# Performance work log

Hardware: AMD Instinct MI355X
Metric: run time of the kernel (lower is better)

Reference implementation:

```python
import jax, jax.numpy as jnp
import numpy as np

HEAD = 4
HW_DIM = 256  # in_dim // 2


def _gconv1x1(x, w, b):
    # groups=2 pointwise conv: x [B,C,H,W], w [O, C//2], b [O]
    B, C, H, W = x.shape
    O = w.shape[0]
    xg = x.reshape(B, 2, C // 2, H, W)
    wg = w.reshape(2, O // 2, C // 2)
    y = jnp.einsum('bgchw,goc->bgohw', xg, wg).reshape(B, O, H, W)
    return y + b[None, :, None, None]


def _bn_train(x, w, b, eps=1e-5):
    # BatchNorm2d in training mode (batch statistics over N,H,W)
    mean = x.mean(axis=(0, 2, 3), keepdims=True)
    var = ((x - mean) ** 2).mean(axis=(0, 2, 3), keepdims=True)
    return (x - mean) / jnp.sqrt(var + eps) * w[None, :, None, None] + b[None, :, None, None]


def _forward(x, wq, bq, wk, bk, wv, bv, bnh_w, bnh_b, bnw_w, bnw_b, gamma):
    B, C, H, W = x.shape
    org_x = x
    # first half of channels is detached in the original forward
    xd = jnp.concatenate([jax.lax.stop_gradient(x[:, :HW_DIM]), x[:, HW_DIM:]], axis=1)

    dqk_h = 512 // HEAD  # 128 per-head qk dim == `long`
    dv_h = 256 // HEAD   # 64 per-head value dim
    q = _gconv1x1(xd, wq, bq).reshape(B, HEAD, dqk_h, H, W)
    k = _gconv1x1(xd, wk, bk).reshape(B, HEAD, dqk_h, H, W)
    v = _gconv1x1(xd, wv, bv).reshape(B, HEAD, dv_h, H, W)
    scale = dqk_h ** (-0.5)

    # --- attention along H (per width column) ---
    eH = jnp.einsum('bnciw,bncjw->bnwij', q, k) * scale  # [B,HEAD,W,H,H]
    aH = jax.nn.softmax(eH, axis=-1)
    out_H = jnp.einsum('bnwij,bncjw->bnciw', aH, v).reshape(B, HEAD * dv_h, H, W)

    # --- attention along W (per height row) ---
    eW = jnp.einsum('bnchi,bnchj->bnhij', q, k) * scale  # [B,HEAD,H,W,W]
    aW = jax.nn.softmax(eW, axis=-1)
    out_W = jnp.einsum('bnhij,bnchj->bnchi', aW, v).reshape(B, HEAD * dv_h, H, W)

    p0 = _bn_train(out_H, bnh_w, bnh_b)[:, :HW_DIM // 2]
    p1 = _bn_train(out_W, bnw_w, bnw_b)[:, :HW_DIM // 2]

    out_temp = jnp.concatenate([out_H, out_W], axis=1)  # pre-BN outputs
    out = gamma * jax.nn.relu(out_temp) + org_x
    return out, p0, p1


def setup_inputs() -> dict:
    key = jax.random.key(0)
    ks = jax.random.split(key, 4)
    B, C, H, W = 4, 512, 128, 128
    s = 0.02
    return {
        'x': jax.random.normal(ks[0], (B, C, H, W), jnp.float32),
        'wq': jax.random.normal(ks[1], (512, 256), jnp.float32) * s,
        'bq': jnp.zeros((512,), jnp.float32),
        'wk': jax.random.normal(ks[2], (512, 256), jnp.float32) * s,
        'bk': jnp.zeros((512,), jnp.float32),
        'wv': jax.random.normal(ks[3], (256, 256), jnp.float32) * s,
        'bv': jnp.zeros((256,), jnp.float32),
        'bnh_w': jnp.ones((256,), jnp.float32),
        'bnh_b': jnp.zeros((256,), jnp.float32),
        'bnw_w': jnp.ones((256,), jnp.float32),
        'bnw_b': jnp.zeros((256,), jnp.float32),
        'gamma': jnp.full((1,), 0.1, jnp.float32),
    }


def reference(x, wq, bq, wk, bk, wv, bv, bnh_w, bnh_b, bnw_w, bnw_b, gamma):
    return _forward(x, wq, bq, wk, bk, wv, bv, bnh_w, bnh_b, bnw_w, bnw_b, gamma)
```

## Files before the change

kernel.cpp:

```cpp
#include <hip/hip_runtime.h>
#include <cstdint>
#include <cstddef>

constexpr int Bn = 4, Cin = 512, Hn = 128, Wn = 128, HWn = Hn * Wn;
constexpr float SCALE_LOG2E = 0.12751743f;
constexpr float INV_CNT = 1.52587890625e-05f;

typedef unsigned short u16;
typedef unsigned int u32;
using f32x4  = __attribute__((ext_vector_type(4))) float;
using bf16x8 = __attribute__((ext_vector_type(8))) short;

#define MFMA(a, b, c) __builtin_amdgcn_mfma_f32_16x16x32_bf16((a), (b), (c), 0, 0, 0)

__device__ __forceinline__ u16 bfu(float f) {
  u32 u = __float_as_uint(f);
  u += 0x7fffu + ((u >> 16) & 1u);
  return (u16)(u >> 16);
}

constexpr size_t SZ_XT = (size_t)Bn * HWn * 512 * 2;
constexpr size_t SZ_QK = (size_t)Bn * 4 * HWn * 128 * 2;
constexpr size_t SZ_V  = (size_t)Bn * 4 * HWn * 64 * 2;
constexpr size_t SZ_O  = (size_t)Bn * 256 * HWn * 4;
constexpr size_t OFF_XT = 0;
constexpr size_t OFF_Q  = OFF_XT + SZ_XT;
constexpr size_t OFF_K  = OFF_Q + SZ_QK;
constexpr size_t OFF_V  = OFF_K + SZ_QK;
constexpr size_t OFF_OH = OFF_V + SZ_V;
constexpr size_t OFF_OW = OFF_OH + SZ_O;
constexpr size_t OFF_ST = OFF_OW + SZ_O;
constexpr size_t OFF_WB = OFF_ST + 4096;
constexpr size_t OFF_BB = OFF_WB + (size_t)1280 * 256 * 2;

__global__ __launch_bounds__(256) void k_transpose_cast(
    const float* __restrict__ x,
    const float* __restrict__ wq, const float* __restrict__ wk, const float* __restrict__ wv,
    const float* __restrict__ bq, const float* __restrict__ bk, const float* __restrict__ bv,
    u16* __restrict__ xT, u16* __restrict__ Wb, float* __restrict__ Bb) {
  __shared__ float tile[32][33];
  const int t = threadIdx.x;
  if (blockIdx.z == 4) {
    if (blockIdx.y == 0 && blockIdx.x < 320) {
      int idx = (blockIdx.x * 256 + t) * 4;
      int row = idx >> 8, col = idx & 255;
      const float* src = (row < 512)  ? (wq + (size_t)row * 256 + col)
                       : (row < 1024) ? (wk + (size_t)(row - 512) * 256 + col)
                                      : (wv + (size_t)(row - 1024) * 256 + col);
      float4 v = *(const float4*)src;
      u32 lo = (u32)bfu(v.x) | ((u32)bfu(v.y) << 16);
      u32 hi = (u32)bfu(v.z) | ((u32)bfu(v.w) << 16);
      *(uint2*)&Wb[idx] = make_uint2(lo, hi);
    } else if (blockIdx.y == 1 && blockIdx.x == 0) {
      for (int i = t; i < 1280; i += 256)
        Bb[i] = (i < 512) ? bq[i] : (i < 1024) ? bk[i - 512] : bv[i - 1024];
    }
    return;
  }
  const int b = blockIdx.z, c0 = blockIdx.y * 32, p0 = blockIdx.x * 32;
  const int pi = t & 31, ci = t >> 5;
  const float* xp = x + ((size_t)b * Cin + c0) * HWn + p0;
  for (int cc = ci; cc < 32; cc += 8) tile[cc][pi] = xp[(size_t)cc * HWn + pi];
  __syncthreads();
  u16* o = xT + ((size_t)b * HWn + p0) * Cin + c0;
  for (int pp = ci; pp < 32; pp += 8) o[(size_t)pp * Cin + pi] = bfu(tile[pi][pp]);
}

__global__ __launch_bounds__(256, 3) void k_proj(
    const u16* __restrict__ xT, const u16* __restrict__ Wb, const float* __restrict__ Bb,
    u16* __restrict__ Q, u16* __restrict__ K, u16* __restrict__ V,
    float* __restrict__ stats) {
  __shared__ u16 xs[128 * 128];

  const int t = threadIdx.x;
  const int ot = blockIdx.x;
  const int pos0 = blockIdx.y * 128;
  const int b = blockIdx.z;

  if (ot == 0 && blockIdx.y == 0 && b == 0) { stats[t] = 0.f; stats[256 + t] = 0.f; }

  const int g = (ot < 8) ? ((ot & 3) >> 1) : (ot - 8);
  const u16* xrow = xT + ((size_t)b * HWn + pos0) * 512 + g * 256;

  const int lane = t & 63, wid = t >> 6, ln = lane & 15, qd = lane >> 4;
  const u16* wr0 = Wb + ((size_t)ot * 128 + wid * 32 + ln) * 256;

  f32x4 acc[2][8];
#pragma unroll
  for (int mi = 0; mi < 2; ++mi)
#pragma unroll
    for (int nt = 0; nt < 8; ++nt) acc[mi][nt] = f32x4{0.f, 0.f, 0.f, 0.f};

  for (int kc = 0; kc < 2; ++kc) {
    __syncthreads();
#pragma unroll
    for (int p = 0; p < 8; ++p) {
      int id = p * 256 + t;
      int pos = id >> 4, kb = id & 15;
      uint4 v = *(const uint4*)(xrow + (size_t)pos * 512 + kc * 128 + kb * 8);
      *(uint4*)&xs[pos * 128 + (kb ^ (pos & 15)) * 8] = v;
    }
    __syncthreads();
    bf16x8 a[2][4];
#pragma unroll
    for (int kk = 0; kk < 4; ++kk) {
      int kbi = kk * 4 + qd;
      a[0][kk] = *(const bf16x8*)(wr0 + kc * 128 + kbi * 8);
      a[1][kk] = *(const bf16x8*)(wr0 + 16 * 256 + kc * 128 + kbi * 8);
    }
#pragma unroll
    for (int kk = 0; kk < 4; ++kk) {
      int kbi = kk * 4 + qd;
#pragma unroll
      for (int nt = 0; nt < 8; ++nt) {
        bf16x8 bf_ = *(const bf16x8*)(xs + (nt * 16 + ln) * 128 + (kbi ^ ln) * 8);
        acc[0][nt] = MFMA(a[0][kk], bf_, acc[0][nt]);
        acc[1][nt] = MFMA(a[1][kk], bf_, acc[1][nt]);
      }
    }
  }
  __syncthreads();
#pragma unroll
  for (int mi = 0; mi < 2; ++mi) {
    int oc = wid * 32 + mi * 16 + qd * 4;
    const float* bp = Bb + ot * 128 + oc;
    float b0 = bp[0], b1 = bp[1], b2 = bp[2], b3 = bp[3];
    int ocb = oc >> 2;
#pragma unroll
    for (int nt = 0; nt < 8; ++nt) {
      int pos = nt * 16 + ln;
      u32 lo = (u32)bfu(acc[mi][nt][0] + b0) | ((u32)bfu(acc[mi][nt][1] + b1) << 16);
      u32 hi = (u32)bfu(acc[mi][nt][2] + b2) | ((u32)bfu(acc[mi][nt][3] + b3) << 16);
      *(uint2*)&xs[pos * 128 + ((ocb ^ (pos & 31)) << 2)] = make_uint2(lo, hi);
    }
  }
  __syncthreads();
  if (ot < 8) {
    u16* dst = (ot < 4) ? Q + (size_t)(b * 4 + ot) * HWn * 128
                        : K + (size_t)(b * 4 + (ot - 4)) * HWn * 128;
#pragma unroll
    for (int p = 0; p < 8; ++p) {
      int id = p * 256 + t;
      int pos = id >> 4, grp = id & 15;
      int s0 = (grp * 2) ^ (pos & 31), s1 = (grp * 2 + 1) ^ (pos & 31);
      uint2 g0 = *(const uint2*)&xs[pos * 128 + (s0 << 2)];
      uint2 g1 = *(const uint2*)&xs[pos * 128 + (s1 << 2)];
      *(uint4*)(dst + (size_t)(pos0 + pos) * 128 + grp * 8) = make_uint4(g0.x, g0.y, g1.x, g1.y);
    }
  } else {
    u16* vb = V + (size_t)(b * 4 + (ot - 8) * 2) * HWn * 64;
#pragma unroll
    for (int p = 0; p < 8; ++p) {
      int id = p * 256 + t;
      int pos = id >> 4, grp = id & 15;
      int off = grp * 8;
      int s0 = (grp * 2) ^ (pos & 31), s1 = (grp * 2 + 1) ^ (pos & 31);
      uint2 g0 = *(const uint2*)&xs[pos * 128 + (s0 << 2)];
      uint2 g1 = *(const uint2*)&xs[pos * 128 + (s1 << 2)];
      u16* d = vb + (size_t)((off >> 6) * HWn + pos0 + pos) * 64 + (off & 63);
      *(uint4*)d = make_uint4(g0.x, g0.y, g1.x, g1.y);
    }
  }
}

__global__ __launch_bounds__(256) void k_attn(
    const u16* __restrict__ Qg, const u16* __restrict__ Kg, const u16* __restrict__ Vg,
    float* __restrict__ outH, float* __restrict__ outW, float* __restrict__ stats) {
  __shared__ u16 sm[64 * 128 + 128 * 128];
  u16* VT = sm;
  u16* KP = sm + 64 * 128;
  float* Os = (float*)KP;
  float* scr = (float*)VT;

  const int t = threadIdx.x;
  const int s = blockIdx.x;
  const int b = blockIdx.y >> 2, n = blockIdx.y & 3;
  const int dir = blockIdx.z;
  const int pos_base = (dir == 0) ? s : s * 128;
  const int step = (dir == 0) ? 128 : 1;

  const u16* qb = Qg + (size_t)(b * 4 + n) * HWn * 128;
  const u16* kb = Kg + (size_t)(b * 4 + n) * HWn * 128;
  const u16* vb = Vg + (size_t)(b * 4 + n) * HWn * 64;

#pragma unroll
  for (int p = 0; p < 8; ++p) {
    int id = p * 256 + t;
    int row = id >> 4, kk = id & 15;
    uint4 v = *(const uint4*)(kb + (size_t)(pos_base + row * step) * 128 + kk * 8);
    *(uint4*)&KP[row * 128 + (kk ^ (row & 15)) * 8] = v;
  }
#pragma unroll
  for (int p = 0; p < 4; ++p) {
    int id = p * 256 + t;
    int j = id >> 3, cb = id & 7;
    uint4 v = *(const uint4*)(vb + (size_t)(pos_base + j * step) * 64 + cb * 8);
    const u16* pv = (const u16*)&v;
    int jb = j >> 3, jr = j & 7;
#pragma unroll
    for (int e = 0; e < 8; ++e) {
      int c = cb * 8 + e;
      VT[c * 128 + (((jb ^ (c & 15)) << 3) | jr)] = pv[e];
    }
  }
  __syncthreads();

  const int lane = t & 63, wid = t >> 6, ln = lane & 15, qd = lane >> 4;
  f32x4 accS[2][8];
#pragma unroll
  for (int mi = 0; mi < 2; ++mi)
#pragma unroll
    for (int nt = 0; nt < 8; ++nt) accS[mi][nt] = f32x4{0.f, 0.f, 0.f, 0.f};

#pragma unroll
  for (int kk = 0; kk < 4; ++kk) {
    int kbi = kk * 4 + qd;
    bf16x8 a0 = *(const bf16x8*)(qb + (size_t)(pos_base + (wid * 32 + ln) * step) * 128 + kbi * 8);
    bf16x8 a1 = *(const bf16x8*)(qb + (size_t)(pos_base + (wid * 32 + 16 + ln) * step) * 128 + kbi * 8);
#pragma unroll
    for (int nt = 0; nt < 8; ++nt) {
      int row = nt * 16 + ln;
      bf16x8 bf_ = *(const bf16x8*)(KP + row * 128 + (kbi ^ ln) * 8);
      accS[0][nt] = MFMA(a0, bf_, accS[0][nt]);
      accS[1][nt] = MFMA(a1, bf_, accS[1][nt]);
    }
  }
  float rinv[2][4];
#pragma unroll
  for (int mi = 0; mi < 2; ++mi)
#pragma unroll
    for (int r = 0; r < 4; ++r) {
      float mx = accS[mi][0][r];
#pragma unroll
      for (int nt = 1; nt < 8; ++nt) mx = fmaxf(mx, accS[mi][nt][r]);
      mx = fmaxf(mx, __shfl_xor(mx, 1));
      mx = fmaxf(mx, __shfl_xor(mx, 2));
      mx = fmaxf(mx, __shfl_xor(mx, 4));
      mx = fmaxf(mx, __shfl_xor(mx, 8));
      float sum = 0.f;
#pragma unroll
      for (int nt = 0; nt < 8; ++nt) {
        float e = exp2f((accS[mi][nt][r] - mx) * SCALE_LOG2E);
        accS[mi][nt][r] = e; sum += e;
      }
      sum += __shfl_xor(sum, 1);
      sum += __shfl_xor(sum, 2);
      sum += __shfl_xor(sum, 4);
      sum += __shfl_xor(sum, 8);
      rinv[mi][r] = __builtin_amdgcn_rcpf(sum);
    }
  __syncthreads();
#pragma unroll
  for (int mi = 0; mi < 2; ++mi) {
    int mbase = (wid * 2 + mi) * 16 + qd * 4;
#pragma unroll
    for (int nt = 0; nt < 8; ++nt) {
      int nb = nt * 2 + (ln >> 3), nr = ln & 7;
#pragma unroll
      for (int r = 0; r < 4; ++r) {
        int m = mbase + r;
        KP[m * 128 + (((nb ^ (m & 15)) << 3) | nr)] = bfu(accS[mi][nt][r]);
      }
    }
  }
  f32x4 accO[2][4];
#pragma unroll
  for (int mi = 0; mi < 2; ++mi)
#pragma unroll
    for (int nt = 0; nt < 4; ++nt) accO[mi][nt] = f32x4{0.f, 0.f, 0.f, 0.f};
#pragma unroll
  for (int jj = 0; jj < 4; ++jj) {
    int jb2 = jj * 4 + qd;
    bf16x8 a0 = *(const bf16x8*)(KP + (wid * 32 + ln) * 128 + (jb2 ^ ln) * 8);
    bf16x8 a1 = *(const bf16x8*)(KP + (wid * 32 + 16 + ln) * 128 + (jb2 ^ ln) * 8);
#pragma unroll
    for (int nt = 0; nt < 4; ++nt) {
      int c = nt * 16 + ln;
      bf16x8 bf_ = *(const bf16x8*)(VT + c * 128 + (jb2 ^ (c & 15)) * 8);
      accO[0][nt] = MFMA(a0, bf_, accO[0][nt]);
      accO[1][nt] = MFMA(a1, bf_, accO[1][nt]);
    }
  }
  __syncthreads();
  float s1[4] = {0.f, 0.f, 0.f, 0.f}, s2[4] = {0.f, 0.f, 0.f, 0.f};
#pragma unroll
  for (int mi = 0; mi < 2; ++mi) {
    int ib = ((wid * 2 + mi) * 16 + qd * 4) >> 2;
#pragma unroll
    for (int nt = 0; nt < 4; ++nt) {
      int c = nt * 16 + ln;
      f32x4 v;
#pragma unroll
      for (int r = 0; r < 4; ++r) v[r] = accO[mi][nt][r] * rinv[mi][r];
      if (n < 2) {
#pragma unroll
        for (int r = 0; r < 4; ++r) { s1[nt] += v[r]; s2[nt] += v[r] * v[r]; }
      }
      *(f32x4*)(Os + c * 128 + ((ib ^ (c & 31)) << 2)) = v;
    }
  }
  if (n < 2) {
#pragma unroll
    for (int nt = 0; nt < 4; ++nt) {
      float a = s1[nt]; a += __shfl_xor(a, 16); a += __shfl_xor(a, 32);
      float q2 = s2[nt]; q2 += __shfl_xor(q2, 16); q2 += __shfl_xor(q2, 32);
      if (qd == 0) {
        scr[(wid * 2 + 0) * 64 + nt * 16 + ln] = a;
        scr[(wid * 2 + 1) * 64 + nt * 16 + ln] = q2;
      }
    }
  }
  __syncthreads();
  if (n < 2 && t < 128) {
    int part = t >> 6, c2 = t & 63;
    float v = scr[(0 * 2 + part) * 64 + c2] + scr[(1 * 2 + part) * 64 + c2] +
              scr[(2 * 2 + part) * 64 + c2] + scr[(3 * 2 + part) * 64 + c2];
    atomicAdd(&stats[dir * 256 + part * 128 + n * 64 + c2], v);
  }
  float* obase; size_t cstride;
  if (dir == 0) { obase = outH + ((size_t)(b * 4 + n) * 128 + s) * 8192; cstride = 128; }
  else          { obase = outW + (size_t)(b * 256 + n * 64) * HWn + (size_t)s * 128; cstride = HWn; }
#pragma unroll
  for (int p = 0; p < 8; ++p) {
    int id = p * 256 + t;
    int c = id >> 5, i4 = id & 31;
    f32x4 v = *(const f32x4*)(Os + c * 128 + ((i4 ^ (c & 31)) << 2));
    *(f32x4*)(obase + (size_t)c * cstride + i4 * 4) = v;
  }
}

__global__ __launch_bounds__(256) void k_final(
    const float* __restrict__ x, const float* __restrict__ outH,
    const float* __restrict__ outW, const float* __restrict__ stats,
    const float* __restrict__ bnh_w, const float* __restrict__ bnh_b,
    const float* __restrict__ bnw_w, const float* __restrict__ bnw_b,
    const float* __restrict__ gamma,
    float* __restrict__ out, float* __restrict__ p0, float* __restrict__ p1) {
  __shared__ float lds[32 * 129];
  const int t = threadIdx.x;
  const int w0 = blockIdx.x * 32;
  const int ch = blockIdx.y;
  const int b = blockIdx.z;
  const float gm = gamma[0];
  const float* xp = x + (size_t)(b * 512 + ch) * HWn;
  float* op = out + (size_t)(b * 512 + ch) * HWn;
  if (ch < 256) {
    const int n = ch >> 6, c = ch & 63;
    const float* hb = outH + (size_t)(b * 4 + n) * 128 * 8192 + c * 128;
    for (int ps = 0; ps < 16; ++ps) {
      int wl = ps * 2 + (t >> 7);
      lds[wl * 129 + (t & 127)] = hb[(size_t)(w0 + wl) * 8192 + (t & 127)];
    }
    __syncthreads();
    const bool dop = ch < 128;
    float mean = 0.f, istd = 0.f, bw = 0.f, bb = 0.f;
    if (dop) {
      mean = stats[ch] * INV_CNT;
      float ex2 = stats[128 + ch] * INV_CNT;
      istd = rsqrtf(fmaxf(ex2 - mean * mean, 0.f) + 1e-5f);
      bw = bnh_w[ch]; bb = bnh_b[ch];
    }
    float* pp = p0 + (size_t)(b * 128 + ch) * HWn;
    const int w = t & 31, h0 = t >> 5;
    for (int hh = 0; hh < 16; ++hh) {
      int h = hh * 8 + h0;
      float v = lds[w * 129 + h];
      int gi = h * 128 + w0 + w;
      op[gi] = gm * fmaxf(v, 0.f) + xp[gi];
      if (dop) pp[gi] = (v - mean) * istd * bw + bb;
    }
  } else {
    const int cw = ch - 256;
    const float* wbp = outW + (size_t)(b * 256 + cw) * HWn;
    const bool dop = cw < 128;
    float mean = 0.f, istd = 0.f, bw = 0.f, bb = 0.f;
    if (dop) {
      mean = stats[256 + cw] * INV_CNT;
      float ex2 = stats[384 + cw] * INV_CNT;
      istd = rsqrtf(fmaxf(ex2 - mean * mean, 0.f) + 1e-5f);
      bw = bnw_w[cw]; bb = bnw_b[cw];
    }
    float* pp = p1 + (size_t)(b * 128 + cw) * HWn;
    for (int it = 0; it < 16; ++it) {
      int fl = it * 256 + t;
      int h = fl >> 5, w = fl & 31;
      int gi = h * 128 + w0 + w;
      float v = wbp[gi];
      op[gi] = gm * fmaxf(v, 0.f) + xp[gi];
      if (dop) pp[gi] = (v - mean) * istd * bw + bb;
    }
  }
}

extern "C" void kernel_launch(void* const* d_in, const int* in_sizes, int n_in,
                              void* d_out, int out_size, void* d_ws, size_t ws_size,
                              hipStream_t stream) {
  (void)in_sizes; (void)n_in; (void)out_size; (void)ws_size;
  const float* x    = (const float*)d_in[0];
  const float* wq   = (const float*)d_in[1];
  const float* bq   = (const float*)d_in[2];
  const float* wk   = (const float*)d_in[3];
  const float* bk   = (const float*)d_in[4];
  const float* wv   = (const float*)d_in[5];
  const float* bv   = (const float*)d_in[6];
  const float* bnhw = (const float*)d_in[7];
  const float* bnhb = (const float*)d_in[8];
  const float* bnww = (const float*)d_in[9];
  const float* bnwb = (const float*)d_in[10];
  const float* gamma = (const float*)d_in[11];

  char* ws = (char*)d_ws;
  u16* xT = (u16*)(ws + OFF_XT);
  u16* Q  = (u16*)(ws + OFF_Q);
  u16* K  = (u16*)(ws + OFF_K);
  u16* V  = (u16*)(ws + OFF_V);
  float* oH = (float*)(ws + OFF_OH);
  float* oW = (float*)(ws + OFF_OW);
  float* st = (float*)(ws + OFF_ST);
  u16* Wb = (u16*)(ws + OFF_WB);
  float* Bb = (float*)(ws + OFF_BB);

  float* out = (float*)d_out;
  float* p0 = out + (size_t)Bn * 512 * HWn;
  float* p1 = p0 + (size_t)Bn * 128 * HWn;

  k_transpose_cast<<<dim3(512, 16, 5), 256, 0, stream>>>(x, wq, wk, wv, bq, bk, bv, xT, Wb, Bb);
  k_proj<<<dim3(10, 128, 4), 256, 0, stream>>>(xT, Wb, Bb, Q, K, V, st);
  k_attn<<<dim3(128, 16, 2), 256, 0, stream>>>(Q, K, V, oH, oW, st);
  k_final<<<dim3(4, 512, 4), 256, 0, stream>>>(x, oH, oW, st, bnhw, bnhb, bnww, bnwb, gamma,
                                               out, p0, p1);
}
```

Before: 577.5 us.

## Fuse W-direction residual epilogue into attention, use direct global-to-LDS loads, remap proj blocks

The W-direction attention now writes the gamma*relu+x output directly and stores raw pre-BN values only for the first 128 channels. The final kernel no longer processes the upper 128 W channels and handles the BN-only path with vectorized loads. K and projection input tiles are copied to LDS with global_load_lds, with the XOR swizzle applied on the global address side. Projection blocks are remapped so neighbouring blocks spread across XCDs. Together these cut HBM traffic for the outW round trip and some register staging, at the cost of more complex index mapping.

```diff
diff --git a/kernel.cpp b/kernel.cpp
--- a/kernel.cpp
+++ b/kernel.cpp
@@ -17,6 +17,12 @@
   u32 u = __float_as_uint(f);
   u += 0x7fffu + ((u >> 16) & 1u);
   return (u16)(u >> 16);
+}
+
+__device__ __forceinline__ void gload_lds16(const void* g, void* l) {
+  __builtin_amdgcn_global_load_lds(
+      (const __attribute__((address_space(1))) u32*)g,
+      (__attribute__((address_space(3))) u32*)l, 16, 0, 0);
 }
 
 constexpr size_t SZ_XT = (size_t)Bn * HWn * 512 * 2;
@@ -73,11 +79,14 @@
   __shared__ u16 xs[128 * 128];
 
   const int t = threadIdx.x;
-  const int ot = blockIdx.x;
-  const int pos0 = blockIdx.y * 128;
-  const int b = blockIdx.z;
-
-  if (ot == 0 && blockIdx.y == 0 && b == 0) { stats[t] = 0.f; stats[256 + t] = 0.f; }
+  const int flat = blockIdx.x + 10 * (blockIdx.y + (blockIdx.z << 7));
+  const int work = ((flat & 7) * 640) + (flat >> 3);
+  const int ot = work % 10;
+  const int rest = work / 10;
+  const int b = rest >> 7;
+  const int pos0 = (rest & 127) << 7;
+
+  if (work == 0) { stats[t] = 0.f; stats[256 + t] = 0.f; }
 
   const int g = (ot < 8) ? ((ot & 3) >> 1) : (ot - 8);
   const u16* xrow = xT + ((size_t)b * HWn + pos0) * 512 + g * 256;
@@ -97,10 +106,9 @@
     for (int p = 0; p < 8; ++p) {
       int id = p * 256 + t;
       int pos = id >> 4, kb = id & 15;
-      uint4 v = *(const uint4*)(xrow + (size_t)pos * 512 + kc * 128 + kb * 8);
-      *(uint4*)&xs[pos * 128 + (kb ^ (pos & 15)) * 8] = v;
-    }
-    __syncthreads();
+      gload_lds16(xrow + (size_t)pos * 512 + kc * 128 + ((kb ^ (pos & 15)) << 3),
+                  xs + id * 8);
+    }
     bf16x8 a[2][4];
 #pragma unroll
     for (int kk = 0; kk < 4; ++kk) {
@@ -108,6 +116,7 @@
       a[0][kk] = *(const bf16x8*)(wr0 + kc * 128 + kbi * 8);
       a[1][kk] = *(const bf16x8*)(wr0 + 16 * 256 + kc * 128 + kbi * 8);
     }
+    __syncthreads();
 #pragma unroll
     for (int kk = 0; kk < 4; ++kk) {
       int kbi = kk * 4 + qd;
@@ -165,7 +174,9 @@
 
 __global__ __launch_bounds__(256) void k_attn(
     const u16* __restrict__ Qg, const u16* __restrict__ Kg, const u16* __restrict__ Vg,
-    float* __restrict__ outH, float* __restrict__ outW, float* __restrict__ stats) {
+    const float* __restrict__ x, const float* __restrict__ gamma,
+    float* __restrict__ outH, float* __restrict__ oWraw, float* __restrict__ out,
+    float* __restrict__ stats) {
   __shared__ u16 sm[64 * 128 + 128 * 128];
   u16* VT = sm;
   u16* KP = sm + 64 * 128;
@@ -187,8 +198,8 @@
   for (int p = 0; p < 8; ++p) {
     int id = p * 256 + t;
     int row = id >> 4, kk = id & 15;
-    uint4 v = *(const uint4*)(kb + (size_t)(pos_base + row * step) * 128 + kk * 8);
-    *(uint4*)&KP[row * 128 + (kk ^ (row & 15)) * 8] = v;
+    gload_lds16(kb + (size_t)(pos_base + row * step) * 128 + ((kk ^ (row & 15)) << 3),
+                KP + id * 8);
   }
 #pragma unroll
   for (int p = 0; p < 4; ++p) {
@@ -317,21 +328,38 @@
               scr[(2 * 2 + part) * 64 + c2] + scr[(3 * 2 + part) * 64 + c2];
     atomicAdd(&stats[dir * 256 + part * 128 + n * 64 + c2], v);
   }
-  float* obase; size_t cstride;
-  if (dir == 0) { obase = outH + ((size_t)(b * 4 + n) * 128 + s) * 8192; cstride = 128; }
-  else          { obase = outW + (size_t)(b * 256 + n * 64) * HWn + (size_t)s * 128; cstride = HWn; }
-#pragma unroll
-  for (int p = 0; p < 8; ++p) {
-    int id = p * 256 + t;
-    int c = id >> 5, i4 = id & 31;
-    f32x4 v = *(const f32x4*)(Os + c * 128 + ((i4 ^ (c & 31)) << 2));
-    *(f32x4*)(obase + (size_t)c * cstride + i4 * 4) = v;
+  if (dir == 0) {
+    float* obase = outH + ((size_t)(b * 4 + n) * 128 + s) * 8192;
+#pragma unroll
+    for (int p = 0; p < 8; ++p) {
+      int id = p * 256 + t;
+      int c = id >> 5, i4 = id & 31;
+      f32x4 v = *(const f32x4*)(Os + c * 128 + ((i4 ^ (c & 31)) << 2));
+      *(f32x4*)(obase + (size_t)c * 128 + i4 * 4) = v;
+    }
+  } else {
+    const float gm = gamma[0];
+    const float* xb = x + ((size_t)b * 512 + 256 + n * 64) * HWn + (size_t)s * 128;
+    float* ob = out + ((size_t)b * 512 + 256 + n * 64) * HWn + (size_t)s * 128;
+    float* rb = oWraw + ((size_t)b * 128 + n * 64) * HWn + (size_t)s * 128;
+#pragma unroll
+    for (int p = 0; p < 8; ++p) {
+      int id = p * 256 + t;
+      int c = id >> 5, i4 = id & 31;
+      f32x4 v = *(const f32x4*)(Os + c * 128 + ((i4 ^ (c & 31)) << 2));
+      f32x4 xv = *(const f32x4*)(xb + (size_t)c * HWn + i4 * 4);
+      f32x4 o;
+#pragma unroll
+      for (int r = 0; r < 4; ++r) o[r] = gm * fmaxf(v[r], 0.f) + xv[r];
+      *(f32x4*)(ob + (size_t)c * HWn + i4 * 4) = o;
+      if (n < 2) *(f32x4*)(rb + (size_t)c * HWn + i4 * 4) = v;
+    }
   }
 }
 
 __global__ __launch_bounds__(256) void k_final(
     const float* __restrict__ x, const float* __restrict__ outH,
-    const float* __restrict__ outW, const float* __restrict__ stats,
+    const float* __restrict__ oWraw, const float* __restrict__ stats,
     const float* __restrict__ bnh_w, const float* __restrict__ bnh_b,
     const float* __restrict__ bnw_w, const float* __restrict__ bnw_b,
     const float* __restrict__ gamma,
@@ -341,10 +369,10 @@
   const int w0 = blockIdx.x * 32;
   const int ch = blockIdx.y;
   const int b = blockIdx.z;
-  const float gm = gamma[0];
-  const float* xp = x + (size_t)(b * 512 + ch) * HWn;
-  float* op = out + (size_t)(b * 512 + ch) * HWn;
   if (ch < 256) {
+    const float gm = gamma[0];
+    const float* xp = x + (size_t)(b * 512 + ch) * HWn;
+    float* op = out + (size_t)(b * 512 + ch) * HWn;
     const int n = ch >> 6, c = ch & 63;
     const float* hb = outH + (size_t)(b * 4 + n) * 128 * 8192 + c * 128;
     for (int ps = 0; ps < 16; ++ps) {
@@ -371,23 +399,19 @@
     }
   } else {
     const int cw = ch - 256;
-    const float* wbp = outW + (size_t)(b * 256 + cw) * HWn;
-    const bool dop = cw < 128;
-    float mean = 0.f, istd = 0.f, bw = 0.f, bb = 0.f;
-    if (dop) {
-      mean = stats[256 + cw] * INV_CNT;
-      float ex2 = stats[384 + cw] * INV_CNT;
-      istd = rsqrtf(fmaxf(ex2 - mean * mean, 0.f) + 1e-5f);
-      bw = bnw_w[cw]; bb = bnw_b[cw];
-    }
-    float* pp = p1 + (size_t)(b * 128 + cw) * HWn;
-    for (int it = 0; it < 16; ++it) {
-      int fl = it * 256 + t;
-      int h = fl >> 5, w = fl & 31;
-      int gi = h * 128 + w0 + w;
-      float v = wbp[gi];
-      op[gi] = gm * fmaxf(v, 0.f) + xp[gi];
-      if (dop) pp[gi] = (v - mean) * istd * bw + bb;
+    const float mean = stats[256 + cw] * INV_CNT;
+    const float ex2 = stats[384 + cw] * INV_CNT;
+    const float istd = rsqrtf(fmaxf(ex2 - mean * mean, 0.f) + 1e-5f);
+    const float bw = bnw_w[cw], bb = bnw_b[cw];
+    const float* rp = oWraw + (size_t)(b * 128 + cw) * HWn + (size_t)blockIdx.x * 4096;
+    float* pp = p1 + (size_t)(b * 128 + cw) * HWn + (size_t)blockIdx.x * 4096;
+#pragma unroll
+    for (int it = 0; it < 4; ++it) {
+      f32x4 v = *(const f32x4*)(rp + (it * 256 + t) * 4);
+      f32x4 o;
+#pragma unroll
+      for (int r = 0; r < 4; ++r) o[r] = (v[r] - mean) * istd * bw + bb;
+      *(f32x4*)(pp + (it * 256 + t) * 4) = o;
     }
   }
 }
@@ -415,7 +439,7 @@
   u16* K  = (u16*)(ws + OFF_K);
   u16* V  = (u16*)(ws + OFF_V);
   float* oH = (float*)(ws + OFF_OH);
-  float* oW = (float*)(ws + OFF_OW);
+  float* oWr = (float*)(ws + OFF_OW);
   float* st = (float*)(ws + OFF_ST);
   u16* Wb = (u16*)(ws + OFF_WB);
   float* Bb = (float*)(ws + OFF_BB);
@@ -426,7 +450,7 @@
 
   k_transpose_cast<<<dim3(512, 16, 5), 256, 0, stream>>>(x, wq, wk, wv, bq, bk, bv, xT, Wb, Bb);
   k_proj<<<dim3(10, 128, 4), 256, 0, stream>>>(xT, Wb, Bb, Q, K, V, st);
-  k_attn<<<dim3(128, 16, 2), 256, 0, stream>>>(Q, K, V, oH, oW, st);
-  k_final<<<dim3(4, 512, 4), 256, 0, stream>>>(x, oH, oW, st, bnhw, bnhb, bnww, bnwb, gamma,
+  k_attn<<<dim3(128, 16, 2), 256, 0, stream>>>(Q, K, V, x, gamma, oH, oWr, out, st);
+  k_final<<<dim3(4, 384, 4), 256, 0, stream>>>(x, oH, oWr, st, bnhw, bnhb, bnww, bnwb, gamma,
                                                out, p0, p1);
 }
```

Measured after the change: 568.7 us. About the same (-1.5%).
